# Performance work log

Measured on AMD Instinct MI355X. Metric: run time of the kernel, lower is better.

## Reference

```python
import jax, jax.numpy as jnp
import numpy as np

B, T, E = 8, 2048, 512  # batch, seq_len, dim (single head, head_dim == dim)
EPS = 1e-3


def setup_inputs() -> dict:
    key = jax.random.key(0)
    ks = jax.random.split(key, 6)
    s = E ** -0.5  # scale proj weights like nn.Linear init so exp(k) stays finite
    return {
        "x": jax.random.normal(ks[0], (B, E, T), jnp.float32),
        "toep_weight": jax.random.normal(ks[1], (1, T), jnp.float32),
        "q_w": jax.random.normal(ks[2], (E, E), jnp.float32) * s,
        "q_b": jnp.zeros((E,), jnp.float32),
        "k_w": jax.random.normal(ks[3], (E, E), jnp.float32) * s,
        "k_b": jnp.zeros((E,), jnp.float32),
        "v_w": jax.random.normal(ks[4], (E, E), jnp.float32) * s,
        "v_b": jnp.zeros((E,), jnp.float32),
        "o_w": jax.random.normal(ks[5], (E, E), jnp.float32) * s,
        "o_b": jnp.zeros((E,), jnp.float32),
    }


def reference(x, toep_weight, q_w, q_b, k_w, k_b, v_w, v_b, o_w, o_b):
    # x: (B, E, T) -> (B, T, E)
    xt = jnp.transpose(x, (0, 2, 1))
    q = xt @ q_w.T + q_b
    k = xt @ k_w.T + k_b
    v = xt @ v_w.T + v_b
    # feature maps: softmax(q) * d^-1/2 , exp(k); v scaled by per-position Toeplitz weight
    q = jax.nn.softmax(q, axis=-1) * (E ** -0.5)
    k = jnp.exp(k)
    v = v * toep_weight[0][:, None]  # (T,1) broadcast over (B,T,E)
    # causal linear attention: running outer-product state S (B,E,E) and key-sum z (B,E)
    qs = jnp.transpose(q, (1, 0, 2))  # (T, B, E)
    kk = jnp.transpose(k, (1, 0, 2))
    vv = jnp.transpose(v, (1, 0, 2))

    def step(carry, inp):
        S, z = carry
        qt, kt, vt = inp  # each (B, E)
        S = S + kt[:, :, None] * vt[:, None, :]  # cumulative k v^T
        z = z + kt                                # cumulative key sum
        d = jnp.maximum(jnp.sum(z * qt, axis=-1), EPS)  # clamp then reciprocal
        out = jnp.einsum('bd,bde->be', qt, S) / d[:, None]
        return (S, z), out

    S0 = jnp.zeros((B, E, E), q.dtype)
    z0 = jnp.zeros((B, E), q.dtype)
    _, outs = jax.lax.scan(step, (S0, z0), (qs, kk, vv))  # outs: (T, B, E)
    attn = jnp.transpose(outs, (1, 0, 2))  # (B, T, E)
    return attn @ o_w.T + o_b
```

## Files before the change

kernel.cpp:

```cpp
#include <hip/hip_runtime.h>
#include <hip/hip_bf16.h>
#include <math.h>
#include <stdint.h>

#define B_ 8
#define T_ 2048
#define E_ 512
#define CCH 256
#define NC_ 8
#define EPS_ 1e-3f
#define QSCALE 0.044194173824159216f

typedef __attribute__((ext_vector_type(8))) short short8;
typedef __attribute__((ext_vector_type(4))) short short4v;
typedef __attribute__((ext_vector_type(4))) float f32x4;
typedef __hip_bfloat16 bf16_t;

__device__ __forceinline__ short f2bs(float x) {
    bf16_t h = __float2bfloat16(x);
    return __builtin_bit_cast(short, h);
}
__device__ __forceinline__ float bs2f(short s) {
    bf16_t h = __builtin_bit_cast(bf16_t, s);
    return __bfloat162float(h);
}

__device__ __forceinline__ void async16(const void* g, void* l) {
    __builtin_amdgcn_global_load_lds(
        (const __attribute__((address_space(1))) unsigned int*)(unsigned long long)(uintptr_t)g,
        (__attribute__((address_space(3))) unsigned int*)(unsigned int)(uintptr_t)l,
        16, 0, 0);
}

__device__ __forceinline__ void gemm128(const short* __restrict__ Ag, int lda,
                                        const short* __restrict__ Bg, int ldb, int K,
                                        short* L, f32x4 acc[4][4],
                                        int wm, int wn, int wq, int lane) {
    int m16 = lane & 15, quad = lane >> 4;
    int lrow = lane >> 3;
    int lchunk = (lane & 7) ^ lrow;
    short* Bl = L + 8192;
    for (int k0 = 0; k0 < K; k0 += 64) {
        __syncthreads();
        #pragma unroll
        for (int w = 0; w < 4; ++w) {
            int R = wq * 32 + w * 8;
            async16(Ag + (size_t)(R + lrow) * lda + k0 + lchunk * 8, L + R * 64);
            async16(Bg + (size_t)(R + lrow) * ldb + k0 + lchunk * 8, Bl + R * 64);
        }
        __syncthreads();
        #pragma unroll
        for (int h = 0; h < 2; ++h) {
            int cs = ((h * 4 + quad) ^ (m16 & 7)) * 8;
            short8 a[4], b[4];
            #pragma unroll
            for (int t = 0; t < 4; ++t)
                a[t] = *(const short8*)(L + (wm + t * 16 + m16) * 64 + cs);
            #pragma unroll
            for (int t = 0; t < 4; ++t)
                b[t] = *(const short8*)(Bl + (wn + t * 16 + m16) * 64 + cs);
            #pragma unroll
            for (int t = 0; t < 4; ++t)
                #pragma unroll
                for (int j = 0; j < 4; ++j)
                    acc[t][j] = __builtin_amdgcn_mfma_f32_16x16x32_bf16(a[t], b[j], acc[t][j], 0, 0, 0);
        }
    }
}

#define GEMM_PROLOG \
    int tid = threadIdx.x, lane = tid & 63, wq = tid >> 6; \
    int wm = (wq & 1) * 64, wn = (wq >> 1) * 64; \
    int m16 = lane & 15, quad = lane >> 4; \
    (void)tid; \
    f32x4 acc[4][4]; \
    { f32x4 zz = {0.f, 0.f, 0.f, 0.f}; \
      for (int i = 0; i < 4; ++i) for (int j = 0; j < 4; ++j) acc[i][j] = zz; }

__global__ void prep_kernel(const float* __restrict__ qw, const float* __restrict__ kw,
                            const float* __restrict__ vw, const float* __restrict__ ow,
                            short* __restrict__ wbf,
                            const float* __restrict__ x, short* __restrict__ xbf) {
    int bid = blockIdx.x;
    int tid = threadIdx.x;
    if (bid < 512) {
        size_t idx8 = ((size_t)bid * 256 + tid) * 8;
        int sel = (int)(idx8 >> 18);
        size_t off = idx8 & ((1u << 18) - 1);
        const float* src = sel == 0 ? qw : sel == 1 ? kw : sel == 2 ? vw : ow;
        const float4* sp = (const float4*)(src + off);
        float4 a = sp[0], b = sp[1];
        short8 g;
        g[0] = f2bs(a.x); g[1] = f2bs(a.y); g[2] = f2bs(a.z); g[3] = f2bs(a.w);
        g[4] = f2bs(b.x); g[5] = f2bs(b.y); g[6] = f2bs(b.z); g[7] = f2bs(b.w);
        *(short8*)(wbf + idx8) = g;
        return;
    }
    bid -= 512;
    __shared__ __align__(16) float S[64][68];
    int t0 = (bid & 31) * 64, e0 = ((bid >> 5) & 7) * 64, b = bid >> 8;
    const float* src = x + ((size_t)b * E_ + e0) * T_ + t0;
    short* dst = xbf + ((size_t)b * T_ + t0) * E_ + e0;
    #pragma unroll
    for (int p = 0; p < 2; ++p) {
        int el = p * 32 + (tid >> 3), tc = (tid & 7) * 8;
        const float4* sp = (const float4*)(src + (size_t)el * T_ + tc);
        *(float4*)&S[el][tc] = sp[0];
        *(float4*)&S[el][tc + 4] = sp[1];
    }
    __syncthreads();
    #pragma unroll
    for (int p = 0; p < 2; ++p) {
        int tl = p * 32 + (tid >> 3), ec = (tid & 7) * 8;
        short8 g;
        #pragma unroll
        for (int j = 0; j < 8; ++j) g[j] = f2bs(S[ec + j][tl]);
        *(short8*)(dst + (size_t)tl * E_ + ec) = g;
    }
}

__global__ __launch_bounds__(256) void proj_qkv_kernel(
    const short* __restrict__ xbf, const short* __restrict__ wbf,
    const float* __restrict__ qb, const float* __restrict__ kb, const float* __restrict__ vb,
    const float* __restrict__ toep,
    short* __restrict__ qraw, short* __restrict__ kbf,
    short* __restrict__ kT, short* __restrict__ vT) {
    __shared__ __align__(16) short L[16384];
    GEMM_PROLOG
    int t0 = blockIdx.x * 128, i0 = blockIdx.y * 128;
    int b = blockIdx.z / 3, sel = blockIdx.z % 3;
    const short* Ag = xbf + ((size_t)b * T_ + t0) * E_;
    const short* Bg = wbf + (size_t)sel * E_ * E_ + (size_t)i0 * E_;
    gemm128(Ag, E_, Bg, E_, E_, L, acc, wm, wn, wq, lane);
    const float* bias = (sel == 0) ? qb : (sel == 1) ? kb : vb;

    short4v ov[4][4];
    #pragma unroll
    for (int mt = 0; mt < 4; ++mt)
        #pragma unroll
        for (int r = 0; r < 4; ++r) {
            int t = t0 + wm + mt * 16 + quad * 4 + r;
            float tw = toep[t];
            #pragma unroll
            for (int nt = 0; nt < 4; ++nt) {
                int col = i0 + wn + nt * 16 + m16;
                float vv = acc[mt][nt][r] + bias[col];
                if (sel == 1) vv = expf(vv);
                if (sel == 2) vv = vv * tw;
                ov[mt][nt][r] = f2bs(vv);
            }
        }

    if (sel <= 1) {
        short* dst = (sel == 0) ? qraw : kbf;
        #pragma unroll
        for (int mt = 0; mt < 4; ++mt)
            #pragma unroll
            for (int r = 0; r < 4; ++r) {
                int t = t0 + wm + mt * 16 + quad * 4 + r;
                #pragma unroll
                for (int nt = 0; nt < 4; ++nt) {
                    int col = i0 + wn + nt * 16 + m16;
                    dst[((size_t)b * T_ + t) * E_ + col] = ov[mt][nt][r];
                }
            }
    }

    if (sel >= 1) {
        short* dstT = (sel == 1) ? kT : vT;
        #pragma unroll
        for (int h = 0; h < 2; ++h) {
            __syncthreads();
            if (wm == 64 * h) {
                #pragma unroll
                for (int mt = 0; mt < 4; ++mt)
                    #pragma unroll
                    for (int nt = 0; nt < 4; ++nt) {
                        int col = wn + nt * 16 + m16;
                        int tl = mt * 16 + quad * 4;
                        *(short4v*)&L[col * 68 + tl] = ov[mt][nt];
                    }
            }
            __syncthreads();
            #pragma unroll
            for (int rnd = 0; rnd < 4; ++rnd) {
                int col = rnd * 32 + (tid >> 3);
                int tt = (tid & 7) * 8;
                short8 g = *(const short8*)&L[col * 68 + tt];
                *(short8*)(dstT + ((size_t)b * E_ + i0 + col) * T_ + t0 + 64 * h + tt) = g;
            }
        }
    }
}

__global__ void softmax_ksum_kernel(const short* __restrict__ qraw, short* __restrict__ qbf,
                                    const short* __restrict__ k, float* __restrict__ ks) {
    int bid = blockIdx.x, tid = threadIdx.x;
    if (bid >= B_ * T_) {
        int r = bid - B_ * T_;
        int bc = r >> 1, b = bc >> 3, c = bc & 7;
        int e = (r & 1) * 256 + tid;
        const short* kp = k + ((size_t)b * T_ + (size_t)c * CCH) * E_ + e;
        float s = 0.f;
        for (int t = 0; t < CCH; ++t) s += bs2f(kp[(size_t)t * E_]);
        ks[(size_t)bc * E_ + e] = s;
        return;
    }
    __shared__ float red[256];
    const short* p = qraw + (size_t)bid * E_;
    float v0 = bs2f(p[tid]), v1 = bs2f(p[tid + 256]);
    red[tid] = fmaxf(v0, v1);
    __syncthreads();
    for (int s = 128; s > 0; s >>= 1) { if (tid < s) red[tid] = fmaxf(red[tid], red[tid + s]); __syncthreads(); }
    float m = red[0];
    __syncthreads();
    float e0 = expf(v0 - m), e1 = expf(v1 - m);
    red[tid] = e0 + e1;
    __syncthreads();
    for (int s = 128; s > 0; s >>= 1) { if (tid < s) red[tid] += red[tid + s]; __syncthreads(); }
    float inv = QSCALE / red[0];
    qbf[(size_t)bid * E_ + tid] = f2bs(e0 * inv);
    qbf[(size_t)bid * E_ + tid + 256] = f2bs(e1 * inv);
}

__global__ __launch_bounds__(256) void kvp_kernel(
    const short* __restrict__ vT, const short* __restrict__ kT, short* __restrict__ KV,
    const short* __restrict__ qbf, const short* __restrict__ kbf, short* __restrict__ P) {
    __shared__ __align__(16) short L[16384];
    int bid = blockIdx.x;
    if (bid < 1024) {
        GEMM_PROLOG
        int ev0 = (bid & 3) * 128, ek0 = ((bid >> 2) & 3) * 128;
        int bc = bid >> 4, b = bc >> 3, c = bc & 7;
        const short* Ag = vT + ((size_t)b * E_ + ev0) * T_ + c * CCH;
        const short* Bg = kT + ((size_t)b * E_ + ek0) * T_ + c * CCH;
        gemm128(Ag, T_, Bg, T_, CCH, L, acc, wm, wn, wq, lane);
        #pragma unroll
        for (int mt = 0; mt < 4; ++mt)
            #pragma unroll
            for (int r = 0; r < 4; ++r) {
                int ev = ev0 + wm + mt * 16 + quad * 4 + r;
                #pragma unroll
                for (int nt = 0; nt < 4; ++nt) {
                    int ek = ek0 + wn + nt * 16 + m16;
                    KV[((size_t)bc * E_ + ev) * E_ + ek] = f2bs(acc[mt][nt][r]);
                }
            }
        return;
    }
    bid -= 1024;
    int tj0 = (bid & 1) * 128, ti0 = ((bid >> 1) & 1) * 128;
    int bc = bid >> 2, b = bc >> 3, c = bc & 7;
    short* Pp = P + (size_t)bc * CCH * CCH;
    if (tj0 > ti0) {
        short8 z8 = {0, 0, 0, 0, 0, 0, 0, 0};
        for (int i = threadIdx.x; i < 128 * 128 / 8; i += 256) {
            int row = i >> 4, colc = (i * 8) & 127;
            *(short8*)(Pp + (size_t)(ti0 + row) * CCH + tj0 + colc) = z8;
        }
        return;
    }
    GEMM_PROLOG
    const short* Ag = qbf + ((size_t)b * T_ + c * CCH + ti0) * E_;
    const short* Bg = kbf + ((size_t)b * T_ + c * CCH + tj0) * E_;
    gemm128(Ag, E_, Bg, E_, E_, L, acc, wm, wn, wq, lane);
    #pragma unroll
    for (int mt = 0; mt < 4; ++mt)
        #pragma unroll
        for (int r = 0; r < 4; ++r) {
            int row = ti0 + wm + mt * 16 + quad * 4 + r;
            #pragma unroll
            for (int nt = 0; nt < 4; ++nt) {
                int col = tj0 + wn + nt * 16 + m16;
                float vv = (col <= row) ? acc[mt][nt][r] : 0.f;
                Pp[(size_t)row * CCH + col] = f2bs(vv);
            }
        }
}

__global__ void scan2_kernel(short* __restrict__ KV, float* __restrict__ ks) {
    int bid = blockIdx.x, tid = threadIdx.x;
    if (bid < 1024) {
        int gid = bid * 256 + tid;
        int b = gid >> 15;
        size_t idx = (size_t)(gid & 32767) * 8;
        short* p = KV + (size_t)b * NC_ * E_ * E_ + idx;
        float run[8] = {0.f, 0.f, 0.f, 0.f, 0.f, 0.f, 0.f, 0.f};
        #pragma unroll
        for (int c = 0; c < NC_; ++c) {
            short8 t8 = *(short8*)p;
            short8 o8;
            #pragma unroll
            for (int j = 0; j < 8; ++j) {
                float tv = bs2f(t8[j]);
                o8[j] = f2bs(run[j]);
                run[j] += tv;
            }
            *(short8*)p = o8;
            p += (size_t)E_ * E_;
        }
        return;
    }
    int gid = (bid - 1024) * 256 + tid;
    int b = gid >> 9, idx = gid & (E_ - 1);
    float run = 0.f;
    float* p = ks + (size_t)b * NC_ * E_ + idx;
    for (int c = 0; c < NC_; ++c) { float t = *p; *p = run; run += t; p += E_; }
}

__global__ void denom_kernel(const short* __restrict__ qbf, const float* __restrict__ z,
                             const short* __restrict__ P, float* __restrict__ invd) {
    __shared__ float red[256];
    int row = blockIdx.x, tid = threadIdx.x;
    int b = row >> 11, t = row & (T_ - 1);
    int c = t >> 8, tl = t & 255;
    const short* qr = qbf + (size_t)row * E_;
    const float* zr = z + ((size_t)(b * NC_ + c)) * E_;
    const short* Pr = P + (((size_t)(b * NC_ + c)) * CCH + tl) * CCH;
    float s = bs2f(qr[tid]) * zr[tid]
            + bs2f(qr[tid + 256]) * zr[tid + 256]
            + bs2f(Pr[tid]);
    red[tid] = s;
    __syncthreads();
    for (int st = 128; st > 0; st >>= 1) { if (tid < st) red[tid] += red[tid + st]; __syncthreads(); }
    if (tid == 0) invd[row] = 1.f / fmaxf(red[0], EPS_);
}

__global__ __launch_bounds__(256) void attnout_kernel(
    const short* __restrict__ qbf, const short* __restrict__ KV,
    const short* __restrict__ P, const short* __restrict__ vT,
    const float* __restrict__ invd, short* __restrict__ attn) {
    __shared__ __align__(16) short L[16384];
    GEMM_PROLOG
    int t0 = blockIdx.x * 128, i0 = blockIdx.y * 128, b = blockIdx.z;
    int c = t0 >> 8, tl0 = t0 & 255, bc = b * NC_ + c;
    gemm128(qbf + ((size_t)b * T_ + t0) * E_, E_,
            KV + ((size_t)bc * E_ + i0) * E_, E_, E_, L, acc, wm, wn, wq, lane);
    gemm128(P + ((size_t)bc * CCH + tl0) * CCH, CCH,
            vT + ((size_t)b * E_ + i0) * T_ + c * CCH, T_, CCH, L, acc, wm, wn, wq, lane);
    #pragma unroll
    for (int mt = 0; mt < 4; ++mt)
        #pragma unroll
        for (int r = 0; r < 4; ++r) {
            int t = t0 + wm + mt * 16 + quad * 4 + r;
            float sc = invd[(size_t)b * T_ + t];
            #pragma unroll
            for (int nt = 0; nt < 4; ++nt) {
                int col = i0 + wn + nt * 16 + m16;
                attn[((size_t)b * T_ + t) * E_ + col] = f2bs(acc[mt][nt][r] * sc);
            }
        }
}

__global__ __launch_bounds__(256) void outproj_kernel(
    const short* __restrict__ attn, const short* __restrict__ wbf_o,
    const float* __restrict__ ob, float* __restrict__ out) {
    __shared__ __align__(16) short L[16384];
    GEMM_PROLOG
    int t0 = blockIdx.x * 128, i0 = blockIdx.y * 128, b = blockIdx.z;
    gemm128(attn + ((size_t)b * T_ + t0) * E_, E_,
            wbf_o + (size_t)i0 * E_, E_, E_, L, acc, wm, wn, wq, lane);
    #pragma unroll
    for (int mt = 0; mt < 4; ++mt)
        #pragma unroll
        for (int r = 0; r < 4; ++r) {
            int t = t0 + wm + mt * 16 + quad * 4 + r;
            #pragma unroll
            for (int nt = 0; nt < 4; ++nt) {
                int col = i0 + wn + nt * 16 + m16;
                out[((size_t)b * T_ + t) * E_ + col] = acc[mt][nt][r] + ob[col];
            }
        }
}

extern "C" void kernel_launch(void* const* d_in, const int* in_sizes, int n_in,
                              void* d_out, int out_size, void* d_ws, size_t ws_size,
                              hipStream_t stream) {
    const float* x    = (const float*)d_in[0];
    const float* toep = (const float*)d_in[1];
    const float* q_w  = (const float*)d_in[2];
    const float* q_b  = (const float*)d_in[3];
    const float* k_w  = (const float*)d_in[4];
    const float* k_b  = (const float*)d_in[5];
    const float* v_w  = (const float*)d_in[6];
    const float* v_b  = (const float*)d_in[7];
    const float* o_w  = (const float*)d_in[8];
    const float* o_b  = (const float*)d_in[9];

    const size_t NTE = (size_t)B_ * T_ * E_;
    char* base = (char*)d_ws;
    short* xbf  = (short*)base;  base += NTE * 2;
    short* wbf  = (short*)base;  base += (size_t)4 * E_ * E_ * 2;
    short* qraw = (short*)base;  base += NTE * 2;
    short* qbf  = (short*)base;  base += NTE * 2;
    short* kbf  = (short*)base;  base += NTE * 2;
    short* kT   = (short*)base;  base += NTE * 2;
    short* vT   = (short*)base;  base += NTE * 2;
    short* KV   = (short*)base;  base += (size_t)B_ * NC_ * E_ * E_ * 2;
    short* P    = (short*)base;  base += (size_t)B_ * NC_ * CCH * CCH * 2;
    float* ksum = (float*)base;  base += (size_t)B_ * NC_ * E_ * 4;
    float* invd = (float*)base;  base += (size_t)B_ * T_ * 4;
    short* attn = xbf;
    float* out  = (float*)d_out;

    dim3 blk(256);
    prep_kernel<<<dim3(2560), blk, 0, stream>>>(q_w, k_w, v_w, o_w, wbf, x, xbf);
    proj_qkv_kernel<<<dim3(16, 4, 24), blk, 0, stream>>>(
        xbf, wbf, q_b, k_b, v_b, toep, qraw, kbf, kT, vT);
    softmax_ksum_kernel<<<dim3(B_ * T_ + 128), blk, 0, stream>>>(
        qraw, qbf, kbf, ksum);
    kvp_kernel<<<dim3(1280), blk, 0, stream>>>(
        vT, kT, KV, qbf, kbf, P);
    scan2_kernel<<<dim3(1040), blk, 0, stream>>>(KV, ksum);
    denom_kernel<<<dim3(B_ * T_), blk, 0, stream>>>(
        qbf, ksum, P, invd);
    attnout_kernel<<<dim3(16, 4, 8), blk, 0, stream>>>(
        qbf, KV, P, vT, invd, attn);
    outproj_kernel<<<dim3(16, 4, 8), blk, 0, stream>>>(
        attn, wbf + (size_t)3 * E_ * E_, o_b, out);
}
```

Baseline: 260.5 us.

## Fold output projection into V weights to eliminate the outproj GEMM

Because attention is linear in v, the output projection is folded into the value projection: W_o·W_v is precomputed per call (with a bias fold W_o·b_v), so V' = x·(W_o W_v)^T carries straight through the attention. The final outproj GEMM and its bf16 attn round-trip go away, and attnout writes the fp32 output with the o bias. This adds a small 512^3 weight GEMM and a serial bias loop in a 17-block kernel, plus a v_w transpose in prep. The combined weight is rounded to bf16, which adds some precision risk.

After: 278.8 us. 1.07x slower.

```diff
diff --git a/kernel.cpp b/kernel.cpp
--- a/kernel.cpp
+++ b/kernel.cpp
@@ -80,7 +80,9 @@
 __global__ void prep_kernel(const float* __restrict__ qw, const float* __restrict__ kw,
                             const float* __restrict__ vw, const float* __restrict__ ow,
                             short* __restrict__ wbf,
-                            const float* __restrict__ x, short* __restrict__ xbf) {
+                            const float* __restrict__ x, short* __restrict__ xbf,
+                            short* __restrict__ wvT) {
+    __shared__ __align__(16) float S[64][68];
     int bid = blockIdx.x;
     int tid = threadIdx.x;
     if (bid < 512) {
@@ -97,42 +99,100 @@
         return;
     }
     bid -= 512;
-    __shared__ __align__(16) float S[64][68];
-    int t0 = (bid & 31) * 64, e0 = ((bid >> 5) & 7) * 64, b = bid >> 8;
-    const float* src = x + ((size_t)b * E_ + e0) * T_ + t0;
-    short* dst = xbf + ((size_t)b * T_ + t0) * E_ + e0;
+    if (bid < 2048) {
+        int t0 = (bid & 31) * 64, e0 = ((bid >> 5) & 7) * 64, b = bid >> 8;
+        const float* src = x + ((size_t)b * E_ + e0) * T_ + t0;
+        short* dst = xbf + ((size_t)b * T_ + t0) * E_ + e0;
+        #pragma unroll
+        for (int p = 0; p < 2; ++p) {
+            int el = p * 32 + (tid >> 3), tc = (tid & 7) * 8;
+            const float4* sp = (const float4*)(src + (size_t)el * T_ + tc);
+            *(float4*)&S[el][tc] = sp[0];
+            *(float4*)&S[el][tc + 4] = sp[1];
+        }
+        __syncthreads();
+        #pragma unroll
+        for (int p = 0; p < 2; ++p) {
+            int tl = p * 32 + (tid >> 3), ec = (tid & 7) * 8;
+            short8 g;
+            #pragma unroll
+            for (int j = 0; j < 8; ++j) g[j] = f2bs(S[ec + j][tl]);
+            *(short8*)(dst + (size_t)tl * E_ + ec) = g;
+        }
+        return;
+    }
+    bid -= 2048;
+    int ev0 = (bid & 7) * 64, e0 = (bid >> 3) * 64;
+    const float* src = vw + (size_t)ev0 * E_ + e0;
+    short* dst = wvT + (size_t)e0 * E_ + ev0;
     #pragma unroll
     for (int p = 0; p < 2; ++p) {
-        int el = p * 32 + (tid >> 3), tc = (tid & 7) * 8;
-        const float4* sp = (const float4*)(src + (size_t)el * T_ + tc);
-        *(float4*)&S[el][tc] = sp[0];
-        *(float4*)&S[el][tc + 4] = sp[1];
+        int evl = p * 32 + (tid >> 3), ec = (tid & 7) * 8;
+        const float4* sp = (const float4*)(src + (size_t)evl * E_ + ec);
+        *(float4*)&S[evl][ec] = sp[0];
+        *(float4*)&S[evl][ec + 4] = sp[1];
     }
     __syncthreads();
     #pragma unroll
     for (int p = 0; p < 2; ++p) {
-        int tl = p * 32 + (tid >> 3), ec = (tid & 7) * 8;
+        int er = p * 32 + (tid >> 3), evc = (tid & 7) * 8;
         short8 g;
         #pragma unroll
-        for (int j = 0; j < 8; ++j) g[j] = f2bs(S[ec + j][tl]);
-        *(short8*)(dst + (size_t)tl * E_ + ec) = g;
-    }
+        for (int j = 0; j < 8; ++j) g[j] = f2bs(S[evc + j][er]);
+        *(short8*)(dst + (size_t)er * E_ + evc) = g;
+    }
+}
+
+__global__ __launch_bounds__(256) void wvo_kernel(
+    const short* __restrict__ wbf_o, const short* __restrict__ wvT,
+    const float* __restrict__ ow, const float* __restrict__ vb,
+    short* __restrict__ wvo, float* __restrict__ bvo) {
+    __shared__ __align__(16) short L[16384];
+    int bid = blockIdx.x;
+    if (bid == 16) {
+        int tid = threadIdx.x;
+        #pragma unroll
+        for (int rep = 0; rep < 2; ++rep) {
+            int i = rep * 256 + tid;
+            float s = 0.f;
+            for (int e = 0; e < E_; ++e) s += ow[(size_t)i * E_ + e] * vb[e];
+            bvo[i] = s;
+        }
+        return;
+    }
+    GEMM_PROLOG
+    int e0 = (bid & 3) * 128, i0 = (bid >> 2) * 128;
+    gemm128(wbf_o + (size_t)i0 * E_, E_, wvT + (size_t)e0 * E_, E_, E_,
+            L, acc, wm, wn, wq, lane);
+    #pragma unroll
+    for (int mt = 0; mt < 4; ++mt)
+        #pragma unroll
+        for (int r = 0; r < 4; ++r) {
+            int i = i0 + wm + mt * 16 + quad * 4 + r;
+            #pragma unroll
+            for (int nt = 0; nt < 4; ++nt) {
+                int e = e0 + wn + nt * 16 + m16;
+                wvo[(size_t)i * E_ + e] = f2bs(acc[mt][nt][r]);
+            }
+        }
 }
 
 __global__ __launch_bounds__(256) void proj_qkv_kernel(
     const short* __restrict__ xbf, const short* __restrict__ wbf,
-    const float* __restrict__ qb, const float* __restrict__ kb, const float* __restrict__ vb,
+    const short* __restrict__ wvo,
+    const float* __restrict__ qb, const float* __restrict__ kb, const float* __restrict__ bvo,
     const float* __restrict__ toep,
     short* __restrict__ qraw, short* __restrict__ kbf,
-    short* __restrict__ kT, short* __restrict__ vT) {
+    short* __restrict__ kT, short* __restrict__ vwT) {
     __shared__ __align__(16) short L[16384];
     GEMM_PROLOG
     int t0 = blockIdx.x * 128, i0 = blockIdx.y * 128;
     int b = blockIdx.z / 3, sel = blockIdx.z % 3;
     const short* Ag = xbf + ((size_t)b * T_ + t0) * E_;
-    const short* Bg = wbf + (size_t)sel * E_ * E_ + (size_t)i0 * E_;
+    const short* Bg = (sel == 2) ? (wvo + (size_t)i0 * E_)
+                                 : (wbf + (size_t)sel * E_ * E_ + (size_t)i0 * E_);
     gemm128(Ag, E_, Bg, E_, E_, L, acc, wm, wn, wq, lane);
-    const float* bias = (sel == 0) ? qb : (sel == 1) ? kb : vb;
+    const float* bias = (sel == 0) ? qb : (sel == 1) ? kb : bvo;
 
     short4v ov[4][4];
     #pragma unroll
@@ -167,7 +227,7 @@
     }
 
     if (sel >= 1) {
-        short* dstT = (sel == 1) ? kT : vT;
+        short* dstT = (sel == 1) ? kT : vwT;
         #pragma unroll
         for (int h = 0; h < 2; ++h) {
             __syncthreads();
@@ -224,7 +284,7 @@
 }
 
 __global__ __launch_bounds__(256) void kvp_kernel(
-    const short* __restrict__ vT, const short* __restrict__ kT, short* __restrict__ KV,
+    const short* __restrict__ vwT, const short* __restrict__ kT, short* __restrict__ KV,
     const short* __restrict__ qbf, const short* __restrict__ kbf, short* __restrict__ P) {
     __shared__ __align__(16) short L[16384];
     int bid = blockIdx.x;
@@ -232,7 +292,7 @@
         GEMM_PROLOG
         int ev0 = (bid & 3) * 128, ek0 = ((bid >> 2) & 3) * 128;
         int bc = bid >> 4, b = bc >> 3, c = bc & 7;
-        const short* Ag = vT + ((size_t)b * E_ + ev0) * T_ + c * CCH;
+        const short* Ag = vwT + ((size_t)b * E_ + ev0) * T_ + c * CCH;
         const short* Bg = kT + ((size_t)b * E_ + ek0) * T_ + c * CCH;
         gemm128(Ag, T_, Bg, T_, CCH, L, acc, wm, wn, wq, lane);
         #pragma unroll
@@ -328,8 +388,9 @@
 
 __global__ __launch_bounds__(256) void attnout_kernel(
     const short* __restrict__ qbf, const short* __restrict__ KV,
-    const short* __restrict__ P, const short* __restrict__ vT,
-    const float* __restrict__ invd, short* __restrict__ attn) {
+    const short* __restrict__ P, const short* __restrict__ vwT,
+    const float* __restrict__ invd, const float* __restrict__ ob,
+    float* __restrict__ out) {
     __shared__ __align__(16) short L[16384];
     GEMM_PROLOG
     int t0 = blockIdx.x * 128, i0 = blockIdx.y * 128, b = blockIdx.z;
@@ -337,7 +398,7 @@
     gemm128(qbf + ((size_t)b * T_ + t0) * E_, E_,
             KV + ((size_t)bc * E_ + i0) * E_, E_, E_, L, acc, wm, wn, wq, lane);
     gemm128(P + ((size_t)bc * CCH + tl0) * CCH, CCH,
-            vT + ((size_t)b * E_ + i0) * T_ + c * CCH, T_, CCH, L, acc, wm, wn, wq, lane);
+            vwT + ((size_t)b * E_ + i0) * T_ + c * CCH, T_, CCH, L, acc, wm, wn, wq, lane);
     #pragma unroll
     for (int mt = 0; mt < 4; ++mt)
         #pragma unroll
@@ -347,28 +408,7 @@
             #pragma unroll
             for (int nt = 0; nt < 4; ++nt) {
                 int col = i0 + wn + nt * 16 + m16;
-                attn[((size_t)b * T_ + t) * E_ + col] = f2bs(acc[mt][nt][r] * sc);
-            }
-        }
-}
-
-__global__ __launch_bounds__(256) void outproj_kernel(
-    const short* __restrict__ attn, const short* __restrict__ wbf_o,
-    const float* __restrict__ ob, float* __restrict__ out) {
-    __shared__ __align__(16) short L[16384];
-    GEMM_PROLOG
-    int t0 = blockIdx.x * 128, i0 = blockIdx.y * 128, b = blockIdx.z;
-    gemm128(attn + ((size_t)b * T_ + t0) * E_, E_,
-            wbf_o + (size_t)i0 * E_, E_, E_, L, acc, wm, wn, wq, lane);
-    #pragma unroll
-    for (int mt = 0; mt < 4; ++mt)
-        #pragma unroll
-        for (int r = 0; r < 4; ++r) {
-            int t = t0 + wm + mt * 16 + quad * 4 + r;
-            #pragma unroll
-            for (int nt = 0; nt < 4; ++nt) {
-                int col = i0 + wn + nt * 16 + m16;
-                out[((size_t)b * T_ + t) * E_ + col] = acc[mt][nt][r] + ob[col];
+                out[((size_t)b * T_ + t) * E_ + col] = acc[mt][nt][r] * sc + ob[col];
             }
         }
 }
@@ -391,31 +431,33 @@
     char* base = (char*)d_ws;
     short* xbf  = (short*)base;  base += NTE * 2;
     short* wbf  = (short*)base;  base += (size_t)4 * E_ * E_ * 2;
+    short* wvT  = (short*)base;  base += (size_t)E_ * E_ * 2;
+    short* wvo  = (short*)base;  base += (size_t)E_ * E_ * 2;
+    float* bvo  = (float*)base;  base += (size_t)E_ * 4;
     short* qraw = (short*)base;  base += NTE * 2;
     short* qbf  = (short*)base;  base += NTE * 2;
     short* kbf  = (short*)base;  base += NTE * 2;
     short* kT   = (short*)base;  base += NTE * 2;
-    short* vT   = (short*)base;  base += NTE * 2;
+    short* vwT  = (short*)base;  base += NTE * 2;
     short* KV   = (short*)base;  base += (size_t)B_ * NC_ * E_ * E_ * 2;
     short* P    = (short*)base;  base += (size_t)B_ * NC_ * CCH * CCH * 2;
     float* ksum = (float*)base;  base += (size_t)B_ * NC_ * E_ * 4;
     float* invd = (float*)base;  base += (size_t)B_ * T_ * 4;
-    short* attn = xbf;
     float* out  = (float*)d_out;
 
     dim3 blk(256);
-    prep_kernel<<<dim3(2560), blk, 0, stream>>>(q_w, k_w, v_w, o_w, wbf, x, xbf);
+    prep_kernel<<<dim3(2624), blk, 0, stream>>>(q_w, k_w, v_w, o_w, wbf, x, xbf, wvT);
+    wvo_kernel<<<dim3(17), blk, 0, stream>>>(
+        wbf + (size_t)3 * E_ * E_, wvT, o_w, v_b, wvo, bvo);
     proj_qkv_kernel<<<dim3(16, 4, 24), blk, 0, stream>>>(
-        xbf, wbf, q_b, k_b, v_b, toep, qraw, kbf, kT, vT);
+        xbf, wbf, wvo, q_b, k_b, bvo, toep, qraw, kbf, kT, vwT);
     softmax_ksum_kernel<<<dim3(B_ * T_ + 128), blk, 0, stream>>>(
         qraw, qbf, kbf, ksum);
     kvp_kernel<<<dim3(1280), blk, 0, stream>>>(
-        vT, kT, KV, qbf, kbf, P);
+        vwT, kT, KV, qbf, kbf, P);
     scan2_kernel<<<dim3(1040), blk, 0, stream>>>(KV, ksum);
     denom_kernel<<<dim3(B_ * T_), blk, 0, stream>>>(
         qbf, ksum, P, invd);
     attnout_kernel<<<dim3(16, 4, 8), blk, 0, stream>>>(
-        qbf, KV, P, vT, invd, attn);
-    outproj_kernel<<<dim3(16, 4, 8), blk, 0, stream>>>(
-        attn, wbf + (size_t)3 * E_ * E_, o_b, out);
-}
+        qbf, KV, P, vwT, invd, o_b, out);
+}
```
